# Performance work log

Measured on AMD Instinct MI355X. Metric: run time of the kernel, lower is better.

## Reference

```python
import jax, jax.numpy as jnp
import numpy as np

CHEB_K = 3
DIM_IN = 2
HIDDEN = 64
EMBED_DIM = 10
NODE_NUM = 2048
BATCH = 32


def _gconv(x, supports, W, b, cheb_k=CHEB_K):
    # Chebyshev graph conv applied directly to x (equivalent to building
    # T_k(A) matrices then applying: T_k(A) x = 2 A T_{k-1}(A) x - T_{k-2}(A) x).
    xs = [x, jnp.einsum('nm,bmc->bnc', supports, x)]
    for _ in range(2, cheb_k):
        xs.append(2.0 * jnp.einsum('nm,bmc->bnc', supports, xs[-1]) - xs[-2])
    x_g = jnp.concatenate(xs, axis=-1)          # [B, N, cheb_k*C]
    return jnp.einsum('bni,io->bno', x_g, W) + b


def setup_inputs() -> dict:
    key = jax.random.key(0)
    ks = jax.random.split(key, 7)
    c_in = DIM_IN + HIDDEN                       # 66
    # xavier_normal-ish scale for weights
    def xavier(k, fan_in, fan_out):
        std = float(np.sqrt(2.0 / (fan_in + fan_out)))
        return jax.random.normal(k, (fan_in, fan_out), dtype=jnp.float32) * std
    return {
        'x': jax.random.normal(ks[0], (BATCH, NODE_NUM, DIM_IN), dtype=jnp.float32),
        'state': jax.random.normal(ks[1], (BATCH, NODE_NUM, HIDDEN), dtype=jnp.float32),
        'node_embeddings': jax.random.normal(ks[2], (NODE_NUM, EMBED_DIM), dtype=jnp.float32),
        'W_gate': xavier(ks[3], CHEB_K * c_in, 2 * HIDDEN),
        'b_gate': jnp.zeros((2 * HIDDEN,), dtype=jnp.float32),
        'W_update': xavier(ks[4], CHEB_K * c_in, HIDDEN),
        'b_update': jnp.zeros((HIDDEN,), dtype=jnp.float32),
    }


def reference(x, state, node_embeddings, W_gate, b_gate, W_update, b_update):
    # adaptive adjacency: softmax(relu(E E^T), axis=1)
    logits = jnp.einsum('nc,mc->nm', node_embeddings, node_embeddings)
    supports = jax.nn.softmax(jax.nn.relu(logits), axis=1)   # [N, N]

    input_and_state = jnp.concatenate([x, state], axis=-1)   # [B, N, dim_in+hidden]
    z_r = jax.nn.sigmoid(_gconv(input_and_state, supports, W_gate, b_gate))
    z, r = jnp.split(z_r, 2, axis=-1)                        # each [B, N, hidden]
    candidate = jnp.concatenate([x, z * state], axis=-1)
    hc = jnp.tanh(_gconv(candidate, supports, W_update, b_update))
    h = r * state + (1.0 - r) * hc
    return h
```

## Files before the change

kernel.cpp:

```cpp
#include <hip/hip_runtime.h>


typedef __bf16 bf16x8 __attribute__((ext_vector_type(8)));
typedef __bf16 bf16x4 __attribute__((ext_vector_type(4)));
typedef float  f32x4  __attribute__((ext_vector_type(4)));

#define GLB(p) ((__attribute__((address_space(1))) void*)(void*)(p))
#define LDS(p) ((__attribute__((address_space(3))) void*)(p))

__global__ void supports_kernel(const float* __restrict__ E, __bf16* __restrict__ S) {
    const int n = blockIdx.x;
    const int t = threadIdx.x;
    const int l = t & 63, w = t >> 6;
    float en[10];
#pragma unroll
    for (int i = 0; i < 10; ++i) en[i] = E[n * 10 + i];
    float vals[8];
    float mx = 0.f;
#pragma unroll
    for (int q = 0; q < 8; ++q) {
        const int m = q * 256 + t;
        const float* em = E + (size_t)m * 10;
        float d = 0.f;
#pragma unroll
        for (int i = 0; i < 10; ++i) d += en[i] * em[i];
        d = fmaxf(d, 0.f);
        vals[q] = d;
        mx = fmaxf(mx, d);
    }
#pragma unroll
    for (int off = 32; off; off >>= 1) mx = fmaxf(mx, __shfl_xor(mx, off));
    __shared__ float sm[4], ss[4];
    if (l == 0) sm[w] = mx;
    __syncthreads();
    mx = fmaxf(fmaxf(sm[0], sm[1]), fmaxf(sm[2], sm[3]));
    float sum = 0.f;
#pragma unroll
    for (int q = 0; q < 8; ++q) { vals[q] = __expf(vals[q] - mx); sum += vals[q]; }
#pragma unroll
    for (int off = 32; off; off >>= 1) sum += __shfl_xor(sum, off);
    if (l == 0) ss[w] = sum;
    __syncthreads();
    sum = ss[0] + ss[1] + ss[2] + ss[3];
    const float inv = 1.f / sum;
#pragma unroll
    for (int q = 0; q < 8; ++q) S[(size_t)n * 2048 + q * 256 + t] = (__bf16)(vals[q] * inv);
}

__global__ __launch_bounds__(256, 2)
void build_t2(const float* __restrict__ x, const float* __restrict__ st,
              const __bf16* __restrict__ zr, __bf16* __restrict__ T) {
    __shared__ float Ls[66 * 129];
    const int b  = blockIdx.x >> 4;
    const int n0 = (blockIdx.x & 15) << 7;
    const int t = threadIdx.x;
    const size_t mb = (size_t)b * 2048 + n0;
    if (t < 128) {
        const float2 v = *(const float2*)&x[(mb + t) * 2];
        Ls[t] = v.x;
        Ls[129 + t] = v.y;
    }
#pragma unroll
    for (int r = 0; r < 8; ++r) {
        const int task = r * 256 + t;
        const int q = task & 15, n = task >> 4;
        f32x4 v = *(const f32x4*)&st[(mb + n) * 64 + q * 4];
        if (zr) {
            const bf16x4 z = *(const bf16x4*)&zr[(mb + n) * 128 + q * 4];
#pragma unroll
            for (int j = 0; j < 4; ++j) v[j] *= (float)z[j];
        }
        const int base = (2 + q * 4) * 129 + n;
#pragma unroll
        for (int j = 0; j < 4; ++j) Ls[base + j * 129] = v[j];
    }
    __syncthreads();
#pragma unroll
    for (int r = 0; r < 5; ++r) {
        const int task = r * 256 + t;
        if (task < 1056) {
            const int c = task >> 4, seg = task & 15;
            const float* src = &Ls[c * 129 + seg * 8];
            bf16x8 o;
#pragma unroll
            for (int j = 0; j < 8; ++j) o[j] = (__bf16)src[j];
            *(bf16x8*)&T[(size_t)(b * 66 + c) * 2048 + n0 + seg * 8] = o;
        }
    }
}

__global__ __launch_bounds__(256, 2)
void transpose_g(const __bf16* __restrict__ T0, const __bf16* __restrict__ T1,
                 const __bf16* __restrict__ T2, __bf16* __restrict__ G) {
    __shared__ __bf16 Ls[128 * 256];
    const int b  = blockIdx.x >> 4;
    const int n0 = (blockIdx.x & 15) << 7;
    const int t = threadIdx.x;
#pragma unroll
    for (int r = 0; r < 14; ++r) {
        const int task = r * 256 + t;
        const int k = task >> 4, seg = task & 15;
        bf16x8 v;
        if (k < 198) {
            const __bf16* T; int c;
            if (k < 66)       { T = T0; c = k; }
            else if (k < 132) { T = T1; c = k - 66; }
            else              { T = T2; c = k - 132; }
            v = *(const bf16x8*)&T[(size_t)(b * 66 + c) * 2048 + n0 + seg * 8];
        } else {
#pragma unroll
            for (int j = 0; j < 8; ++j) v[j] = (__bf16)0.f;
        }
        const int base = seg * 8 * 256 + (((k >> 3) ^ seg) << 3) + (k & 7);
#pragma unroll
        for (int j = 0; j < 8; ++j) Ls[base + j * 256] = v[j];
    }
    __syncthreads();
#pragma unroll
    for (int r = 0; r < 16; ++r) {
        const int task = r * 256 + t;
        const int m = task >> 5, c8 = task & 31;
        if (c8 < 28) {
            bf16x8 w = *(const bf16x8*)&Ls[m * 256 + ((c8 ^ (m >> 3)) << 3)];
            *(bf16x8*)&G[(size_t)(b * 2048 + n0 + m) * 224 + c8 * 8] = w;
        }
    }
}

__global__ void build_wt(const float* __restrict__ W, __bf16* __restrict__ WT, int Nout) {
    const int id = blockIdx.x * 256 + threadIdx.x;
    if (id >= 128 * 224) return;
    const int o = id / 224, k = id % 224;
    WT[id] = (o < Nout && k < 198) ? (__bf16)W[(size_t)k * Nout + o] : (__bf16)0.f;
}

__global__ __launch_bounds__(256, 4)
void gemm_bt(const __bf16* __restrict__ A, int lda,
             const __bf16* __restrict__ Bt, int ldb,
             int K, int epi,
             __bf16* __restrict__ outT, const __bf16* __restrict__ subT,
             float* __restrict__ outF, const float* __restrict__ bias,
             __bf16* __restrict__ zrO, const __bf16* __restrict__ zrI,
             const float* __restrict__ state) {
    __shared__ __bf16 As[64 * 32];
    __shared__ __bf16 Bs[64 * 32];
    const int t = threadIdx.x;
    const int l = t & 63, w = t >> 6;
    const int wr = w >> 1, wc = w & 1;
    const int m0 = blockIdx.x * 64;
    const int n0 = blockIdx.y * 64;
    const int lm = l & 15;
    const int lk = (l >> 4) * 8;
    const int srow = t >> 2;
    const int skc = (t & 3) * 8;

    f32x4 acc[2][2];
#pragma unroll
    for (int i = 0; i < 2; ++i)
#pragma unroll
        for (int j = 0; j < 2; ++j) acc[i][j] = (f32x4)0.f;

    const __bf16* Ab = A + (size_t)(m0 + srow) * lda + skc;
    const __bf16* Bb = Bt + (size_t)(n0 + srow) * ldb + skc;
    __bf16* AsD = As + t * 8;
    __bf16* BsD = Bs + t * 8;

    for (int k0 = 0; k0 < K; k0 += 32) {
        __builtin_amdgcn_global_load_lds(GLB(Ab + k0), LDS(AsD), 16, 0, 0);
        __builtin_amdgcn_global_load_lds(GLB(Bb + k0), LDS(BsD), 16, 0, 0);
        __syncthreads();
        bf16x8 af[2], bfr[2];
#pragma unroll
        for (int i = 0; i < 2; ++i)
            af[i] = *(const bf16x8*)(As + (wr * 32 + i * 16 + lm) * 32 + lk);
#pragma unroll
        for (int j = 0; j < 2; ++j)
            bfr[j] = *(const bf16x8*)(Bs + (wc * 32 + j * 16 + lm) * 32 + lk);
#pragma unroll
        for (int i = 0; i < 2; ++i)
#pragma unroll
            for (int j = 0; j < 2; ++j)
                acc[i][j] = __builtin_amdgcn_mfma_f32_16x16x32_bf16(af[i], bfr[j], acc[i][j], 0, 0, 0);
        __syncthreads();
    }

    const int rb0 = m0 + wr * 32 + (l >> 4) * 4;
    const int cb0 = n0 + wc * 32 + lm;
#pragma unroll
    for (int i = 0; i < 2; ++i) {
        const int rbase = rb0 + i * 16;
#pragma unroll
        for (int j = 0; j < 2; ++j) {
            const int c = cb0 + j * 16;
            f32x4 v = acc[i][j];
            if (epi == 0) {
                bf16x4 pk;
#pragma unroll
                for (int r = 0; r < 4; ++r) pk[r] = (__bf16)v[r];
                *(bf16x4*)&outT[(size_t)c * 2048 + rbase] = pk;
            } else if (epi == 1) {
                bf16x4 s = *(const bf16x4*)&subT[(size_t)c * 2048 + rbase];
                bf16x4 pk;
#pragma unroll
                for (int r = 0; r < 4; ++r) pk[r] = (__bf16)(2.f * v[r] - (float)s[r]);
                *(bf16x4*)&outT[(size_t)c * 2048 + rbase] = pk;
            } else if (epi == 2) {
                const float bb = bias[c];
#pragma unroll
                for (int r = 0; r < 4; ++r) {
                    float xx = fminf(fmaxf(v[r] + bb, -30.f), 30.f);
                    zrO[(size_t)(rbase + r) * 128 + c] = (__bf16)(1.f / (1.f + __expf(-xx)));
                }
            } else {
                const float bb = bias[c];
#pragma unroll
                for (int r = 0; r < 4; ++r) {
                    const int m = rbase + r;
                    float xx = fminf(fmaxf(v[r] + bb, -15.f), 15.f);
                    float e = __expf(2.f * xx);
                    float hc = (e - 1.f) / (e + 1.f);
                    float rr = (float)zrI[(size_t)m * 128 + 64 + c];
                    float s = state[(size_t)m * 64 + c];
                    outF[(size_t)m * 64 + c] = rr * s + (1.f - rr) * hc;
                }
            }
        }
    }
}

extern "C" void kernel_launch(void* const* d_in, const int* in_sizes, int n_in,
                              void* d_out, int out_size, void* d_ws, size_t ws_size,
                              hipStream_t stream) {
    (void)in_sizes; (void)n_in; (void)out_size; (void)ws_size;
    const float* x  = (const float*)d_in[0];
    const float* st = (const float*)d_in[1];
    const float* E  = (const float*)d_in[2];
    const float* Wg = (const float*)d_in[3];
    const float* bg = (const float*)d_in[4];
    const float* Wu = (const float*)d_in[5];
    const float* bu = (const float*)d_in[6];
    float* out = (float*)d_out;

    char* p = (char*)d_ws;
    __bf16* S   = (__bf16*)p; p += (size_t)2048 * 2048 * 2;
    __bf16* T0  = (__bf16*)p; p += (size_t)2112 * 2048 * 2;
    __bf16* T1  = (__bf16*)p; p += (size_t)2112 * 2048 * 2;
    __bf16* T2  = (__bf16*)p; p += (size_t)2112 * 2048 * 2;
    __bf16* G   = (__bf16*)p; p += (size_t)65536 * 224 * 2;
    __bf16* ZR  = (__bf16*)p; p += (size_t)65536 * 128 * 2;
    __bf16* WTg = (__bf16*)p; p += 128 * 224 * 2;
    __bf16* WTu = (__bf16*)p; p += 128 * 224 * 2;

    build_wt<<<112, 256, 0, stream>>>(Wg, WTg, 128);
    build_wt<<<112, 256, 0, stream>>>(Wu, WTu, 64);
    supports_kernel<<<2048, 256, 0, stream>>>(E, S);

    build_t2<<<512, 256, 0, stream>>>(x, st, nullptr, T0);
    gemm_bt<<<dim3(32, 33), 256, 0, stream>>>(S, 2048, T0, 2048, 2048, 0, T1, nullptr, nullptr, nullptr, nullptr, nullptr, nullptr);
    gemm_bt<<<dim3(32, 33), 256, 0, stream>>>(S, 2048, T1, 2048, 2048, 1, T2, T0, nullptr, nullptr, nullptr, nullptr, nullptr);
    transpose_g<<<512, 256, 0, stream>>>(T0, T1, T2, G);
    gemm_bt<<<dim3(1024, 2), 256, 0, stream>>>(G, 224, WTg, 224, 224, 2, nullptr, nullptr, nullptr, bg, ZR, nullptr, nullptr);

    build_t2<<<512, 256, 0, stream>>>(x, st, ZR, T0);
    gemm_bt<<<dim3(32, 33), 256, 0, stream>>>(S, 2048, T0, 2048, 2048, 0, T1, nullptr, nullptr, nullptr, nullptr, nullptr, nullptr);
    gemm_bt<<<dim3(32, 33), 256, 0, stream>>>(S, 2048, T1, 2048, 2048, 1, T2, T0, nullptr, nullptr, nullptr, nullptr, nullptr);
    transpose_g<<<512, 256, 0, stream>>>(T0, T1, T2, G);
    gemm_bt<<<dim3(1024, 1), 256, 0, stream>>>(G, 224, WTu, 224, 224, 3, nullptr, nullptr, out, bu, nullptr, ZR, st);
}
```

Baseline: 313.9 us.

## Replace GEMM with larger 64x128 tile, K=64 swizzled LDS kernel

Replaces the 64x64 tile, K=32 GEMM with a 128-thread kernel that computes 64x128 output tiles over K steps of 64. It uses an XOR-swizzled LDS layout to avoid bank conflicts and gives each wave a 4x4 grid of MFMA accumulators. Buffers are padded to multiples of 128 columns (T to 2176 rows, G and WT to K=256), and a zero_pad kernel clears the extra rows. The goal is more data reuse per load and fewer redundant reads of S across column blocks. The cost is more padded work, fewer waves per CU, and more registers per thread.

```diff
diff --git a/kernel.cpp b/kernel.cpp
--- a/kernel.cpp
+++ b/kernel.cpp
@@ -45,6 +45,14 @@
     const float inv = 1.f / sum;
 #pragma unroll
     for (int q = 0; q < 8; ++q) S[(size_t)n * 2048 + q * 256 + t] = (__bf16)(vals[q] * inv);
+}
+
+__global__ void zero_pad(__bf16* __restrict__ Tpad) {
+    const int id = blockIdx.x * 256 + threadIdx.x;
+    bf16x8 z;
+#pragma unroll
+    for (int j = 0; j < 8; ++j) z[j] = (__bf16)0.f;
+    *(bf16x8*)&Tpad[(size_t)id * 8] = z;
 }
 
 __global__ __launch_bounds__(256, 2)
@@ -97,7 +105,7 @@
     const int n0 = (blockIdx.x & 15) << 7;
     const int t = threadIdx.x;
 #pragma unroll
-    for (int r = 0; r < 14; ++r) {
+    for (int r = 0; r < 16; ++r) {
         const int task = r * 256 + t;
         const int k = task >> 4, seg = task & 15;
         bf16x8 v;
@@ -120,77 +128,83 @@
     for (int r = 0; r < 16; ++r) {
         const int task = r * 256 + t;
         const int m = task >> 5, c8 = task & 31;
-        if (c8 < 28) {
-            bf16x8 w = *(const bf16x8*)&Ls[m * 256 + ((c8 ^ (m >> 3)) << 3)];
-            *(bf16x8*)&G[(size_t)(b * 2048 + n0 + m) * 224 + c8 * 8] = w;
-        }
+        bf16x8 w = *(const bf16x8*)&Ls[m * 256 + ((c8 ^ (m >> 3)) << 3)];
+        *(bf16x8*)&G[(size_t)(b * 2048 + n0 + m) * 256 + c8 * 8] = w;
     }
 }
 
 __global__ void build_wt(const float* __restrict__ W, __bf16* __restrict__ WT, int Nout) {
     const int id = blockIdx.x * 256 + threadIdx.x;
-    if (id >= 128 * 224) return;
-    const int o = id / 224, k = id % 224;
+    const int o = id >> 8, k = id & 255;
     WT[id] = (o < Nout && k < 198) ? (__bf16)W[(size_t)k * Nout + o] : (__bf16)0.f;
 }
 
-__global__ __launch_bounds__(256, 4)
-void gemm_bt(const __bf16* __restrict__ A, int lda,
-             const __bf16* __restrict__ Bt, int ldb,
-             int K, int epi,
-             __bf16* __restrict__ outT, const __bf16* __restrict__ subT,
-             float* __restrict__ outF, const float* __restrict__ bias,
-             __bf16* __restrict__ zrO, const __bf16* __restrict__ zrI,
-             const float* __restrict__ state) {
-    __shared__ __bf16 As[64 * 32];
-    __shared__ __bf16 Bs[64 * 32];
+__global__ __launch_bounds__(128, 3)
+void gemm_s(const __bf16* __restrict__ A, int lda,
+            const __bf16* __restrict__ Bt, int ldb,
+            int K, int epi,
+            __bf16* __restrict__ outT, const __bf16* __restrict__ subT,
+            float* __restrict__ outF, const float* __restrict__ bias,
+            __bf16* __restrict__ zrO, const __bf16* __restrict__ zrI,
+            const float* __restrict__ state) {
+    __shared__ __align__(16) __bf16 As[64 * 64];
+    __shared__ __align__(16) __bf16 Bs[128 * 64];
     const int t = threadIdx.x;
     const int l = t & 63, w = t >> 6;
-    const int wr = w >> 1, wc = w & 1;
+    const int lm = l & 15, kq = l >> 4;
+    const int lm7 = lm & 7;
     const int m0 = blockIdx.x * 64;
-    const int n0 = blockIdx.y * 64;
-    const int lm = l & 15;
-    const int lk = (l >> 4) * 8;
-    const int srow = t >> 2;
-    const int skc = (t & 3) * 8;
-
-    f32x4 acc[2][2];
-#pragma unroll
-    for (int i = 0; i < 2; ++i)
-#pragma unroll
-        for (int j = 0; j < 2; ++j) acc[i][j] = (f32x4)0.f;
-
-    const __bf16* Ab = A + (size_t)(m0 + srow) * lda + skc;
-    const __bf16* Bb = Bt + (size_t)(n0 + srow) * ldb + skc;
-    __bf16* AsD = As + t * 8;
-    __bf16* BsD = Bs + t * 8;
-
-    for (int k0 = 0; k0 < K; k0 += 32) {
-        __builtin_amdgcn_global_load_lds(GLB(Ab + k0), LDS(AsD), 16, 0, 0);
-        __builtin_amdgcn_global_load_lds(GLB(Bb + k0), LDS(BsD), 16, 0, 0);
+    const int c0 = blockIdx.y * 128;
+    const int sr = l >> 3;
+    const int gsw = (l & 7) ^ sr;
+
+    f32x4 acc[4][4];
+#pragma unroll
+    for (int i = 0; i < 4; ++i)
+#pragma unroll
+        for (int j = 0; j < 4; ++j) acc[i][j] = (f32x4)0.f;
+
+    const __bf16* Asrc = A  + (size_t)(m0 + w * 32 + sr) * lda + gsw * 8;
+    const __bf16* Bsrc = Bt + (size_t)(c0 + w * 64 + sr) * ldb + gsw * 8;
+    __bf16* AsD = As + (w * 32) * 64 + l * 8;
+    __bf16* BsD = Bs + (w * 64) * 64 + l * 8;
+
+    for (int k0 = 0; k0 < K; k0 += 64) {
+#pragma unroll
+        for (int q = 0; q < 4; ++q)
+            __builtin_amdgcn_global_load_lds(GLB(Asrc + (size_t)q * 8 * lda + k0),
+                                             LDS(AsD + q * 8 * 64), 16, 0, 0);
+#pragma unroll
+        for (int q = 0; q < 8; ++q)
+            __builtin_amdgcn_global_load_lds(GLB(Bsrc + (size_t)q * 8 * ldb + k0),
+                                             LDS(BsD + q * 8 * 64), 16, 0, 0);
         __syncthreads();
-        bf16x8 af[2], bfr[2];
-#pragma unroll
-        for (int i = 0; i < 2; ++i)
-            af[i] = *(const bf16x8*)(As + (wr * 32 + i * 16 + lm) * 32 + lk);
-#pragma unroll
-        for (int j = 0; j < 2; ++j)
-            bfr[j] = *(const bf16x8*)(Bs + (wc * 32 + j * 16 + lm) * 32 + lk);
-#pragma unroll
-        for (int i = 0; i < 2; ++i)
-#pragma unroll
-            for (int j = 0; j < 2; ++j)
-                acc[i][j] = __builtin_amdgcn_mfma_f32_16x16x32_bf16(af[i], bfr[j], acc[i][j], 0, 0, 0);
+#pragma unroll
+        for (int ks = 0; ks < 2; ++ks) {
+            const int ga = (((ks << 2) | kq) ^ lm7) << 3;
+            bf16x8 af[4], bfr[4];
+#pragma unroll
+            for (int i = 0; i < 4; ++i)
+                af[i] = *(const bf16x8*)(As + (i * 16 + lm) * 64 + ga);
+#pragma unroll
+            for (int j = 0; j < 4; ++j)
+                bfr[j] = *(const bf16x8*)(Bs + (w * 64 + j * 16 + lm) * 64 + ga);
+#pragma unroll
+            for (int i = 0; i < 4; ++i)
+#pragma unroll
+                for (int j = 0; j < 4; ++j)
+                    acc[i][j] = __builtin_amdgcn_mfma_f32_16x16x32_bf16(af[i], bfr[j], acc[i][j], 0, 0, 0);
+        }
         __syncthreads();
     }
 
-    const int rb0 = m0 + wr * 32 + (l >> 4) * 4;
-    const int cb0 = n0 + wc * 32 + lm;
-#pragma unroll
-    for (int i = 0; i < 2; ++i) {
+    const int rb0 = m0 + kq * 4;
+    const int cb0 = c0 + w * 64 + lm;
+#pragma unroll
+    for (int i = 0; i < 4; ++i) {
         const int rbase = rb0 + i * 16;
 #pragma unroll
-        for (int j = 0; j < 2; ++j) {
+        for (int j = 0; j < 4; ++j) {
             const int c = cb0 + j * 16;
             f32x4 v = acc[i][j];
             if (epi == 0) {
@@ -212,16 +226,18 @@
                     zrO[(size_t)(rbase + r) * 128 + c] = (__bf16)(1.f / (1.f + __expf(-xx)));
                 }
             } else {
-                const float bb = bias[c];
-#pragma unroll
-                for (int r = 0; r < 4; ++r) {
-                    const int m = rbase + r;
-                    float xx = fminf(fmaxf(v[r] + bb, -15.f), 15.f);
-                    float e = __expf(2.f * xx);
-                    float hc = (e - 1.f) / (e + 1.f);
-                    float rr = (float)zrI[(size_t)m * 128 + 64 + c];
-                    float s = state[(size_t)m * 64 + c];
-                    outF[(size_t)m * 64 + c] = rr * s + (1.f - rr) * hc;
+                if (c < 64) {
+                    const float bb = bias[c];
+#pragma unroll
+                    for (int r = 0; r < 4; ++r) {
+                        const int m = rbase + r;
+                        float xx = fminf(fmaxf(v[r] + bb, -15.f), 15.f);
+                        float e = __expf(2.f * xx);
+                        float hc = (e - 1.f) / (e + 1.f);
+                        float rr = (float)zrI[(size_t)m * 128 + 64 + c];
+                        float s = state[(size_t)m * 64 + c];
+                        outF[(size_t)m * 64 + c] = rr * s + (1.f - rr) * hc;
+                    }
                 }
             }
         }
@@ -243,27 +259,28 @@
 
     char* p = (char*)d_ws;
     __bf16* S   = (__bf16*)p; p += (size_t)2048 * 2048 * 2;
-    __bf16* T0  = (__bf16*)p; p += (size_t)2112 * 2048 * 2;
-    __bf16* T1  = (__bf16*)p; p += (size_t)2112 * 2048 * 2;
-    __bf16* T2  = (__bf16*)p; p += (size_t)2112 * 2048 * 2;
-    __bf16* G   = (__bf16*)p; p += (size_t)65536 * 224 * 2;
+    __bf16* T0  = (__bf16*)p; p += (size_t)2176 * 2048 * 2;
+    __bf16* T1  = (__bf16*)p; p += (size_t)2176 * 2048 * 2;
+    __bf16* T2  = (__bf16*)p; p += (size_t)2176 * 2048 * 2;
+    __bf16* G   = (__bf16*)p; p += (size_t)65536 * 256 * 2;
     __bf16* ZR  = (__bf16*)p; p += (size_t)65536 * 128 * 2;
-    __bf16* WTg = (__bf16*)p; p += 128 * 224 * 2;
-    __bf16* WTu = (__bf16*)p; p += 128 * 224 * 2;
-
-    build_wt<<<112, 256, 0, stream>>>(Wg, WTg, 128);
-    build_wt<<<112, 256, 0, stream>>>(Wu, WTu, 64);
+    __bf16* WTg = (__bf16*)p; p += 128 * 256 * 2;
+    __bf16* WTu = (__bf16*)p; p += 128 * 256 * 2;
+
+    build_wt<<<128, 256, 0, stream>>>(Wg, WTg, 128);
+    build_wt<<<128, 256, 0, stream>>>(Wu, WTu, 64);
+    zero_pad<<<64, 256, 0, stream>>>(T0 + (size_t)2112 * 2048);
     supports_kernel<<<2048, 256, 0, stream>>>(E, S);
 
     build_t2<<<512, 256, 0, stream>>>(x, st, nullptr, T0);
-    gemm_bt<<<dim3(32, 33), 256, 0, stream>>>(S, 2048, T0, 2048, 2048, 0, T1, nullptr, nullptr, nullptr, nullptr, nullptr, nullptr);
-    gemm_bt<<<dim3(32, 33), 256, 0, stream>>>(S, 2048, T1, 2048, 2048, 1, T2, T0, nullptr, nullptr, nullptr, nullptr, nullptr);
+    gemm_s<<<dim3(32, 17), 128, 0, stream>>>(S, 2048, T0, 2048, 2048, 0, T1, nullptr, nullptr, nullptr, nullptr, nullptr, nullptr);
+    gemm_s<<<dim3(32, 17), 128, 0, stream>>>(S, 2048, T1, 2048, 2048, 1, T2, T0, nullptr, nullptr, nullptr, nullptr, nullptr);
     transpose_g<<<512, 256, 0, stream>>>(T0, T1, T2, G);
-    gemm_bt<<<dim3(1024, 2), 256, 0, stream>>>(G, 224, WTg, 224, 224, 2, nullptr, nullptr, nullptr, bg, ZR, nullptr, nullptr);
+    gemm_s<<<dim3(1024, 1), 128, 0, stream>>>(G, 256, WTg, 256, 256, 2, nullptr, nullptr, nullptr, bg, ZR, nullptr, nullptr);
 
     build_t2<<<512, 256, 0, stream>>>(x, st, ZR, T0);
-    gemm_bt<<<dim3(32, 33), 256, 0, stream>>>(S, 2048, T0, 2048, 2048, 0, T1, nullptr, nullptr, nullptr, nullptr, nullptr, nullptr);
-    gemm_bt<<<dim3(32, 33), 256, 0, stream>>>(S, 2048, T1, 2048, 2048, 1, T2, T0, nullptr, nullptr, nullptr, nullptr, nullptr);
+    gemm_s<<<dim3(32, 17), 128, 0, stream>>>(S, 2048, T0, 2048, 2048, 0, T1, nullptr, nullptr, nullptr, nullptr, nullptr, nullptr);
+    gemm_s<<<dim3(32, 17), 128, 0, stream>>>(S, 2048, T1, 2048, 2048, 1, T2, T0, nullptr, nullptr, nullptr, nullptr, nullptr);
     transpose_g<<<512, 256, 0, stream>>>(T0, T1, T2, G);
-    gemm_bt<<<dim3(1024, 1), 256, 0, stream>>>(G, 224, WTu, 224, 224, 3, nullptr, nullptr, out, bu, nullptr, ZR, st);
-}
+    gemm_s<<<dim3(1024, 1), 128, 0, stream>>>(G, 256, WTu, 256, 256, 3, nullptr, nullptr, out, bu, nullptr, ZR, st);
+}
```

After: 297.3 us. -5.3%, faster.
